# Performance work log

Measured on AMD Instinct MI355X. Metric: run time of the kernel, lower is better.

## Reference

```python
import jax, jax.numpy as jnp
import numpy as np

N_NODES = 50000
N_EDGES = 800000
D = 128


def _graph_conv(x, W, b, src, dst, n_nodes):
    """DGL GraphConv with norm='both': D_in^{-1/2} A D_out^{-1/2} X W + b."""
    ones = jnp.ones((src.shape[0],), dtype=x.dtype)
    out_deg = jax.ops.segment_sum(ones, src, num_segments=n_nodes)
    in_deg = jax.ops.segment_sum(ones, dst, num_segments=n_nodes)
    out_norm = jax.lax.rsqrt(jnp.maximum(out_deg, 1.0))  # [N]
    in_norm = jax.lax.rsqrt(jnp.maximum(in_deg, 1.0))    # [N]
    # scale src features, transform (in_feats == out_feats so order is free), aggregate
    h = (x * out_norm[:, None]) @ W                       # [N, D]
    msgs = h[src]                                         # [E, D] gather
    agg = jax.ops.segment_sum(msgs, dst, num_segments=n_nodes)  # [N, D] scatter-add
    return agg * in_norm[:, None] + b


def setup_inputs() -> dict:
    key = jax.random.key(0)
    ks = jax.random.split(key, 8)
    x = jax.random.normal(ks[0], (N_NODES, D), dtype=jnp.float32)
    src = jax.random.randint(ks[1], (N_EDGES,), 0, N_NODES, dtype=jnp.int64)
    dst = jax.random.randint(ks[2], (N_EDGES,), 0, N_NODES, dtype=jnp.int64)
    scale = 1.0 / np.sqrt(D)
    W1 = jax.random.normal(ks[3], (D, D), dtype=jnp.float32) * scale
    W2 = jax.random.normal(ks[4], (D, D), dtype=jnp.float32) * scale
    W3 = jax.random.normal(ks[5], (D, D), dtype=jnp.float32) * scale
    b1 = jnp.zeros((D,), dtype=jnp.float32)
    b2 = jnp.zeros((D,), dtype=jnp.float32)
    b3 = jnp.zeros((D,), dtype=jnp.float32)
    return {"x": x, "src": src, "dst": dst,
            "W1": W1, "b1": b1, "W2": W2, "b2": b2, "W3": W3, "b3": b3}


def reference(x, src, dst, W1, b1, W2, b2, W3, b3):
    h = _graph_conv(x, W1, b1, src, dst, N_NODES)
    h = jax.nn.relu(h)
    h = _graph_conv(h, W2, b2, src, dst, N_NODES)
    h = jax.nn.relu(h)
    h = _graph_conv(h, W3, b3, src, dst, N_NODES)
    return h
```

## Files before the change

### kernel.cpp

```cpp
#include <hip/hip_runtime.h>
#include <hip/hip_fp16.h>

#define D 128
#define HB 128
#define HT 1024
#define WMAX 12800

struct alignas(16) H8 { __half2 h[4]; };
typedef _Float16 v8h __attribute__((ext_vector_type(8)));
typedef float v4f __attribute__((ext_vector_type(4)));

__global__ __launch_bounds__(HT) void hist_kernel(const int* __restrict__ src,
                                                  const int* __restrict__ dst,
                                                  unsigned* __restrict__ partial_out,
                                                  unsigned* __restrict__ partial_in,
                                                  unsigned char* __restrict__ lrank,
                                                  int nE, int W, int epb) {
    __shared__ unsigned lcnt[WMAX];
    const bool is_dst = (blockIdx.x < HB);
    const int b = is_dst ? blockIdx.x : (blockIdx.x - HB);
    const int t = threadIdx.x;
    for (int i = t; i < W; i += HT) lcnt[i] = 0;
    __syncthreads();
    const int e0 = b * epb;
    const int e1 = min(nE, e0 + epb);
    if (is_dst) {
        for (int e = e0 + t; e < e1; e += HT) {
            const int d = dst[e];
            const unsigned sh = (unsigned)(d & 3) * 8u;
            const unsigned old = atomicAdd(&lcnt[d >> 2], 1u << sh);
            lrank[e] = (unsigned char)((old >> sh) & 0xffu);
        }
    } else {
        for (int e = e0 + t; e < e1; e += HT) {
            const int s = src[e];
            atomicAdd(&lcnt[s >> 2], 1u << ((unsigned)(s & 3) * 8u));
        }
    }
    __syncthreads();
    unsigned* g = (is_dst ? partial_in : partial_out) + (size_t)b * W;
    for (int i = t; i < W; i += HT) g[i] = lcnt[i];
}

__global__ __launch_bounds__(256) void reduce_hist_kernel(const unsigned* __restrict__ partial_out,
                                                          const unsigned* __restrict__ partial_in,
                                                          unsigned* __restrict__ offs_in,
                                                          int* __restrict__ cnt_out,
                                                          int* __restrict__ cnt_in,
                                                          int W, int n, int nbW) {
    const bool is_dst = ((int)blockIdx.x < nbW);
    const int w = (is_dst ? blockIdx.x : (blockIdx.x - nbW)) * 256 + threadIdx.x;
    if (w >= W) return;
    unsigned run = 0;
    if (is_dst) {
#pragma unroll 16
        for (int b = 0; b < HB; ++b) {
            const unsigned c = partial_in[(size_t)b * W + w];
            offs_in[(size_t)b * W + w] = run;
            run += c;
        }
    } else {
#pragma unroll 16
        for (int b = 0; b < HB; ++b) run += partial_out[(size_t)b * W + w];
    }
    int* cnt = is_dst ? cnt_in : cnt_out;
    const int n0 = w * 4;
    const int4 c4 = make_int4((int)(run & 0xffu), (int)((run >> 8) & 0xffu),
                              (int)((run >> 16) & 0xffu), (int)((run >> 24) & 0xffu));
    if (n0 + 3 < n) {
        *(int4*)&cnt[n0] = c4;
    } else {
        const int* cp = &c4.x;
        for (int i = 0; i < 4 && n0 + i < n; ++i) cnt[n0 + i] = cp[i];
    }
}

__global__ __launch_bounds__(1024) void scan_block_kernel(const int* __restrict__ deg,
                                                          int* __restrict__ rp,
                                                          int* __restrict__ bsum, int n) {
    __shared__ int wsum[16];
    const int t = threadIdx.x;
    const int lane = t & 63;
    const int wid = t >> 6;
    const int i = blockIdx.x * 1024 + t;
    const int v = (i < n) ? deg[i] : 0;
    int s = v;
#pragma unroll
    for (int off = 1; off < 64; off <<= 1) {
        int u = __shfl_up(s, off, 64);
        if (lane >= off) s += u;
    }
    if (lane == 63) wsum[wid] = s;
    __syncthreads();
    if (wid == 0) {
        int ws = (lane < 16) ? wsum[lane] : 0;
#pragma unroll
        for (int off = 1; off < 16; off <<= 1) {
            int u = __shfl_up(ws, off, 64);
            if (lane >= off) ws += u;
        }
        if (lane < 16) wsum[lane] = ws;
    }
    __syncthreads();
    const int excl = s - v + ((wid > 0) ? wsum[wid - 1] : 0);
    if (i < n) rp[i] = excl;
    if (t == 0) bsum[blockIdx.x] = wsum[15];
}

__global__ __launch_bounds__(1024) void finalize_kernel(int* __restrict__ rp,
                                                        const int* __restrict__ bsum,
                                                        const int* __restrict__ cnt_out,
                                                        const int* __restrict__ cnt_in,
                                                        float* __restrict__ onorm,
                                                        float* __restrict__ inorm,
                                                        int n, int nb, int nE) {
    __shared__ int prefix_s;
    const int t = threadIdx.x;
    if (t < 64) {
        int v = (t < nb && t < (int)blockIdx.x) ? bsum[t] : 0;
#pragma unroll
        for (int off = 1; off < 64; off <<= 1) v += __shfl_xor(v, off, 64);
        if (t == 0) prefix_s = v;
    }
    __syncthreads();
    const int i = blockIdx.x * 1024 + t;
    if (i < n) {
        rp[i] += prefix_s;
        onorm[i] = rsqrtf(fmaxf((float)cnt_out[i], 1.0f));
        inorm[i] = rsqrtf(fmaxf((float)cnt_in[i], 1.0f));
    }
    if (blockIdx.x == 0 && t == 0) rp[n] = nE;
}

__global__ void fill_csr_kernel(const int* __restrict__ src, const int* __restrict__ dst,
                                const unsigned char* __restrict__ lrank,
                                const unsigned* __restrict__ offs_in,
                                const int* __restrict__ rp,
                                int* __restrict__ srcs_sorted, int nE, int epb, int W) {
    const int e = blockIdx.x * 256 + threadIdx.x;
    if (e < nE) {
        const int d = dst[e];
        const int b = e / epb;
        const unsigned off = (offs_in[(size_t)b * W + (d >> 2)] >> ((unsigned)(d & 3) * 8u)) & 0xffu;
        srcs_sorted[rp[d] + (int)off + (int)lrank[e]] = src[e];
    }
}

__global__ __launch_bounds__(256) void prep_w_kernel(const float* __restrict__ W1,
                                                     const float* __restrict__ W2,
                                                     const float* __restrict__ W3,
                                                     _Float16* __restrict__ wt) {
    const int l = blockIdx.x;
    const float* Wsrc = (l == 0) ? W1 : ((l == 1) ? W2 : W3);
    _Float16* o = wt + (size_t)l * D * D;
    for (int i = threadIdx.x; i < D * D; i += 256) {
        const int k = i >> 7, n = i & 127;
        o[n * D + k] = (_Float16)Wsrc[i];
    }
}

template <bool EPI>
__global__ __launch_bounds__(256) void aggregate_kernel(const __half* __restrict__ xh,
                                                        const float* __restrict__ onorm,
                                                        const float* __restrict__ inorm,
                                                        const float* __restrict__ bias,
                                                        const int* __restrict__ rp,
                                                        const int* __restrict__ srcs,
                                                        __half* __restrict__ agg, int n_nodes) {
    const int node = blockIdx.x * 4 + (threadIdx.x >> 6);
    const int lane = threadIdx.x & 63;
    const int rg = lane >> 4;
    const int c8 = lane & 15;
    if (node >= n_nodes) return;
    const int e0 = rp[node];
    const int e1 = rp[node + 1];

    float acc0[8], acc1[8];
#pragma unroll
    for (int j = 0; j < 8; ++j) { acc0[j] = 0.f; acc1[j] = 0.f; }

    auto accum = [&](float* acc, const H8 v) {
#pragma unroll
        for (int j = 0; j < 4; ++j) {
            acc[2 * j]     += __low2float(v.h[j]);
            acc[2 * j + 1] += __high2float(v.h[j]);
        }
    };

    int e = e0;
    for (; e + 16 <= e1; e += 16) {
        const int s0 = srcs[e + rg];
        const int s1 = srcs[e + 4 + rg];
        const int s2 = srcs[e + 8 + rg];
        const int s3 = srcs[e + 12 + rg];
        const H8 v0 = ((const H8*)(xh + (size_t)s0 * D))[c8];
        const H8 v1 = ((const H8*)(xh + (size_t)s1 * D))[c8];
        const H8 v2 = ((const H8*)(xh + (size_t)s2 * D))[c8];
        const H8 v3 = ((const H8*)(xh + (size_t)s3 * D))[c8];
        accum(acc0, v0); accum(acc1, v1); accum(acc0, v2); accum(acc1, v3);
    }
    for (; e + 4 <= e1; e += 4) {
        const int s0 = srcs[e + rg];
        accum(acc0, ((const H8*)(xh + (size_t)s0 * D))[c8]);
    }
    if (e < e1 && rg < (e1 - e)) {
        const int s0 = srcs[e + rg];
        accum(acc1, ((const H8*)(xh + (size_t)s0 * D))[c8]);
    }

    float r[8];
#pragma unroll
    for (int j = 0; j < 8; ++j) r[j] = acc0[j] + acc1[j];
#pragma unroll
    for (int off = 16; off < 64; off <<= 1)
#pragma unroll
        for (int j = 0; j < 8; ++j) r[j] += __shfl_xor(r[j], off, 64);

    if (rg == 0) {
        if (EPI) {
            const float inm = inorm[node];
            const float onm = onorm[node];
            const float4 bv0 = ((const float4*)bias)[c8 * 2];
            const float4 bv1 = ((const float4*)bias)[c8 * 2 + 1];
            const float* bp0 = &bv0.x;
            const float* bp1 = &bv1.x;
#pragma unroll
            for (int j = 0; j < 4; ++j) {
                r[j]     = fmaxf(fmaf(r[j],     inm, bp0[j]), 0.f) * onm;
                r[j + 4] = fmaxf(fmaf(r[j + 4], inm, bp1[j]), 0.f) * onm;
            }
        }
        H8 h;
#pragma unroll
        for (int j = 0; j < 4; ++j) h.h[j] = __floats2half2_rn(r[2 * j], r[2 * j + 1]);
        ((H8*)(agg + (size_t)node * D))[c8] = h;
    }
}

template <bool A16, bool FULL, bool RELU, bool OSCALE, bool OUT16>
__global__ __launch_bounds__(256) void gemm_mfma_kernel(const void* __restrict__ Av,
                                                        const _Float16* __restrict__ Wt,
                                                        const float* __restrict__ bias,
                                                        const float* __restrict__ inorm,
                                                        const float* __restrict__ onorm,
                                                        void* __restrict__ outv, int nrows) {
    __shared__ _Float16 sA[128 * 136];
    __shared__ _Float16 sB[128 * 136];
    const int t = threadIdx.x;
    const int row0 = blockIdx.x * 128;
    const int rr = t >> 4;
    const int c8 = t & 15;

#pragma unroll
    for (int pass = 0; pass < 8; ++pass) {
        const int row = pass * 16 + rr;
        *(float4*)&sB[row * 136 + c8 * 8] = *(const float4*)&Wt[(size_t)row * D + c8 * 8];
        const int grow = row0 + row;
        if (A16) {
            float4 v = make_float4(0.f, 0.f, 0.f, 0.f);
            if (grow < nrows)
                v = *(const float4*)((const _Float16*)Av + (size_t)grow * D + c8 * 8);
            *(float4*)&sA[row * 136 + c8 * 8] = v;
        } else {
            float4 u0 = make_float4(0.f, 0.f, 0.f, 0.f);
            float4 u1 = u0;
            if (grow < nrows) {
                const float* ap = (const float*)Av + (size_t)grow * D + c8 * 8;
                u0 = ((const float4*)ap)[0];
                u1 = ((const float4*)ap)[1];
            }
            v8h hv;
            hv[0] = (_Float16)u0.x; hv[1] = (_Float16)u0.y;
            hv[2] = (_Float16)u0.z; hv[3] = (_Float16)u0.w;
            hv[4] = (_Float16)u1.x; hv[5] = (_Float16)u1.y;
            hv[6] = (_Float16)u1.z; hv[7] = (_Float16)u1.w;
            *(v8h*)&sA[row * 136 + c8 * 8] = hv;
        }
    }
    __syncthreads();

    const int w = t >> 6;
    const int lane = t & 63;
    const int m16 = lane & 15;
    const int quad = lane >> 4;

    v4f c[2][8];
#pragma unroll
    for (int rt = 0; rt < 2; ++rt)
#pragma unroll
        for (int ct = 0; ct < 8; ++ct) c[rt][ct] = (v4f){0.f, 0.f, 0.f, 0.f};

#pragma unroll
    for (int ks = 0; ks < 4; ++ks) {
        v8h afr[2], bfr[8];
#pragma unroll
        for (int rt = 0; rt < 2; ++rt)
            afr[rt] = *(const v8h*)&sA[(w * 32 + rt * 16 + m16) * 136 + ks * 32 + quad * 8];
#pragma unroll
        for (int ct = 0; ct < 8; ++ct)
            bfr[ct] = *(const v8h*)&sB[(ct * 16 + m16) * 136 + ks * 32 + quad * 8];
#pragma unroll
        for (int rt = 0; rt < 2; ++rt)
#pragma unroll
            for (int ct = 0; ct < 8; ++ct)
                c[rt][ct] = __builtin_amdgcn_mfma_f32_16x16x32_f16(afr[rt], bfr[ct], c[rt][ct], 0, 0, 0);
    }

#pragma unroll
    for (int rt = 0; rt < 2; ++rt) {
#pragma unroll
        for (int r = 0; r < 4; ++r) {
            const int row = row0 + w * 32 + rt * 16 + quad * 4 + r;
            if (row < nrows) {
                const float inm = FULL ? inorm[row] : 1.0f;
                const float osc = OSCALE ? onorm[row] : 1.0f;
#pragma unroll
                for (int ct = 0; ct < 8; ++ct) {
                    const int col = ct * 16 + m16;
                    float v = c[rt][ct][r];
                    if (FULL) v = fmaf(v, inm, bias[col]);
                    if (RELU) v = fmaxf(v, 0.f);
                    if (OSCALE) v *= osc;
                    if (OUT16) ((__half*)outv)[(size_t)row * D + col] = __float2half(v);
                    else       ((float*)outv)[(size_t)row * D + col] = v;
                }
            }
        }
    }
}

extern "C" void kernel_launch(void* const* d_in, const int* in_sizes, int n_in,
                              void* d_out, int out_size, void* d_ws, size_t ws_size,
                              hipStream_t stream) {
    const float* x   = (const float*)d_in[0];
    const int*   src = (const int*)d_in[1];
    const int*   dst = (const int*)d_in[2];
    const float* W1  = (const float*)d_in[3];
    const float* b1  = (const float*)d_in[4];
    const float* W2  = (const float*)d_in[5];
    const float* b2  = (const float*)d_in[6];
    const float* W3  = (const float*)d_in[7];
    const float* b3  = (const float*)d_in[8];

    const int N = in_sizes[0] / D;
    const int E = in_sizes[1];

    char* p = (char*)d_ws;
    auto alloc = [&](size_t bytes) -> void* {
        void* r = (void*)p;
        p += (bytes + 255) & ~(size_t)255;
        return r;
    };
    int*           cnt_out = (int*)alloc((size_t)N * 4);
    int*           cnt_in  = (int*)alloc((size_t)N * 4);
    int*           rp      = (int*)alloc((size_t)(N + 1) * 4);
    int*           bsum    = (int*)alloc(1024 * 4);
    float*         onorm   = (float*)alloc((size_t)N * 4);
    float*         inorm   = (float*)alloc((size_t)N * 4);
    int*           srcs    = (int*)alloc((size_t)E * 4);
    unsigned char* lrank   = (unsigned char*)alloc((size_t)E);
    _Float16*      wt      = (_Float16*)alloc((size_t)3 * D * D * 2);
    __half*        hbuf0   = (__half*)alloc((size_t)N * D * 2);
    __half*        hbuf1   = (__half*)alloc((size_t)N * D * 2);
    char*          scratch = (char*)alloc((size_t)3 * HB * ((N + 3) / 4) * 4);

    const int W = (N + 3) / 4;
    const int epb = (E + HB - 1) / HB;
    unsigned* partial_in  = (unsigned*)scratch;
    unsigned* partial_out = partial_in + (size_t)HB * W;
    unsigned* offs_in     = partial_out + (size_t)HB * W;
    __half*   abuf        = (__half*)scratch;
    float*    outf        = (float*)d_out;

    const int nb = (N + 1023) / 1024;
    const int nbW = (W + 255) / 256;
    const int gemmGrid = (N + 127) / 128;
    const int edgeGrid = (E + 255) / 256;
    const int aggGrid = (N + 3) / 4;

    prep_w_kernel<<<3, 256, 0, stream>>>(W1, W2, W3, wt);
    hist_kernel<<<2 * HB, HT, 0, stream>>>(src, dst, partial_out, partial_in, lrank, E, W, epb);
    reduce_hist_kernel<<<2 * nbW, 256, 0, stream>>>(partial_out, partial_in, offs_in,
                                                    cnt_out, cnt_in, W, N, nbW);
    scan_block_kernel<<<nb, 1024, 0, stream>>>(cnt_in, rp, bsum, N);
    finalize_kernel<<<nb, 1024, 0, stream>>>(rp, bsum, cnt_out, cnt_in, onorm, inorm, N, nb, E);
    fill_csr_kernel<<<edgeGrid, 256, 0, stream>>>(src, dst, lrank, offs_in, rp, srcs, E, epb, W);

    gemm_mfma_kernel<false, false, false, true, true><<<gemmGrid, 256, 0, stream>>>(
        x, wt, b1, inorm, onorm, hbuf0, N);
    aggregate_kernel<true><<<aggGrid, 256, 0, stream>>>(
        hbuf0, onorm, inorm, b1, rp, srcs, hbuf1, N);
    aggregate_kernel<false><<<aggGrid, 256, 0, stream>>>(
        hbuf1, onorm, inorm, b2, rp, srcs, abuf, N);
    gemm_mfma_kernel<true, true, true, true, true><<<gemmGrid, 256, 0, stream>>>(
        abuf, wt + (size_t)D * D, b2, inorm, onorm, hbuf0, N);
    aggregate_kernel<false><<<aggGrid, 256, 0, stream>>>(
        hbuf0, onorm, inorm, b3, rp, srcs, abuf, N);
    gemm_mfma_kernel<true, true, false, false, false><<<gemmGrid, 256, 0, stream>>>(
        abuf, wt + (size_t)2 * D * D, b3, inorm, onorm, outf, N);
}
```

Measured before the change: 262.2 us.

## Merge weight prep into histogram kernel and fuse CSR fill with first GEMM

Weight transpose/convert now runs as three extra blocks of the histogram launch, and the CSR fill runs as extra blocks inside a new 1024-thread first-layer GEMM kernel. This removes two kernel launches and lets the scatter fill overlap with the first dense transform. The new GEMM uses 16 waves per block, each computing a 16x64 tile. Output is written per element as scalar half stores instead of vectorized stores, and 1024-thread blocks with 68KB of shared memory may limit occupancy.

```diff
diff --git a/kernel.cpp b/kernel.cpp
--- a/kernel.cpp
+++ b/kernel.cpp
@@ -15,11 +15,25 @@
                                                   unsigned* __restrict__ partial_out,
                                                   unsigned* __restrict__ partial_in,
                                                   unsigned char* __restrict__ lrank,
+                                                  const float* __restrict__ W1,
+                                                  const float* __restrict__ W2,
+                                                  const float* __restrict__ W3,
+                                                  _Float16* __restrict__ wt,
                                                   int nE, int W, int epb) {
+    const int t = threadIdx.x;
+    if ((int)blockIdx.x >= 2 * HB) {
+        const int l = blockIdx.x - 2 * HB;
+        const float* Wsrc = (l == 0) ? W1 : ((l == 1) ? W2 : W3);
+        _Float16* o = wt + (size_t)l * D * D;
+        for (int i = t; i < D * D; i += HT) {
+            const int k = i >> 7, n = i & 127;
+            o[n * D + k] = (_Float16)Wsrc[i];
+        }
+        return;
+    }
     __shared__ unsigned lcnt[WMAX];
     const bool is_dst = (blockIdx.x < HB);
     const int b = is_dst ? blockIdx.x : (blockIdx.x - HB);
-    const int t = threadIdx.x;
     for (int i = t; i < W; i += HT) lcnt[i] = 0;
     __syncthreads();
     const int e0 = b * epb;
@@ -132,30 +146,85 @@
     if (blockIdx.x == 0 && t == 0) rp[n] = nE;
 }
 
-__global__ void fill_csr_kernel(const int* __restrict__ src, const int* __restrict__ dst,
-                                const unsigned char* __restrict__ lrank,
-                                const unsigned* __restrict__ offs_in,
-                                const int* __restrict__ rp,
-                                int* __restrict__ srcs_sorted, int nE, int epb, int W) {
-    const int e = blockIdx.x * 256 + threadIdx.x;
-    if (e < nE) {
-        const int d = dst[e];
-        const int b = e / epb;
-        const unsigned off = (offs_in[(size_t)b * W + (d >> 2)] >> ((unsigned)(d & 3) * 8u)) & 0xffu;
-        srcs_sorted[rp[d] + (int)off + (int)lrank[e]] = src[e];
-    }
-}
-
-__global__ __launch_bounds__(256) void prep_w_kernel(const float* __restrict__ W1,
-                                                     const float* __restrict__ W2,
-                                                     const float* __restrict__ W3,
-                                                     _Float16* __restrict__ wt) {
-    const int l = blockIdx.x;
-    const float* Wsrc = (l == 0) ? W1 : ((l == 1) ? W2 : W3);
-    _Float16* o = wt + (size_t)l * D * D;
-    for (int i = threadIdx.x; i < D * D; i += 256) {
-        const int k = i >> 7, n = i & 127;
-        o[n * D + k] = (_Float16)Wsrc[i];
+__global__ __launch_bounds__(1024) void gemm1_fill_kernel(
+    const float* __restrict__ x, const _Float16* __restrict__ wt,
+    const float* __restrict__ onorm, __half* __restrict__ y1, int nrows,
+    const int* __restrict__ src, const int* __restrict__ dst,
+    const unsigned char* __restrict__ lrank, const unsigned* __restrict__ offs_in,
+    const int* __restrict__ rp, int* __restrict__ srcs_sorted,
+    int nE, int epb, int W, int nGemmBlocks) {
+    __shared__ _Float16 sA[128 * 136];
+    __shared__ _Float16 sB[128 * 136];
+    const int t = threadIdx.x;
+
+    if ((int)blockIdx.x >= nGemmBlocks) {
+        const int e = (blockIdx.x - nGemmBlocks) * 1024 + t;
+        if (e < nE) {
+            const int d = dst[e];
+            const int b = e / epb;
+            const unsigned off =
+                (offs_in[(size_t)b * W + (d >> 2)] >> ((unsigned)(d & 3) * 8u)) & 0xffu;
+            srcs_sorted[rp[d] + (int)off + (int)lrank[e]] = src[e];
+        }
+        return;
+    }
+
+    const int row0 = blockIdx.x * 128;
+    const int rr = t >> 4;
+    const int c8 = t & 15;
+#pragma unroll
+    for (int pass = 0; pass < 2; ++pass) {
+        const int row = pass * 64 + rr;
+        *(float4*)&sB[row * 136 + c8 * 8] = *(const float4*)&wt[(size_t)row * D + c8 * 8];
+        const int grow = row0 + row;
+        float4 u0 = make_float4(0.f, 0.f, 0.f, 0.f);
+        float4 u1 = u0;
+        if (grow < nrows) {
+            const float* ap = x + (size_t)grow * D + c8 * 8;
+            u0 = ((const float4*)ap)[0];
+            u1 = ((const float4*)ap)[1];
+        }
+        v8h hv;
+        hv[0] = (_Float16)u0.x; hv[1] = (_Float16)u0.y;
+        hv[2] = (_Float16)u0.z; hv[3] = (_Float16)u0.w;
+        hv[4] = (_Float16)u1.x; hv[5] = (_Float16)u1.y;
+        hv[6] = (_Float16)u1.z; hv[7] = (_Float16)u1.w;
+        *(v8h*)&sA[row * 136 + c8 * 8] = hv;
+    }
+    __syncthreads();
+
+    const int w = t >> 6;
+    const int lane = t & 63;
+    const int m16 = lane & 15;
+    const int quad = lane >> 4;
+    const int rt = w >> 1;
+    const int ch = w & 1;
+
+    v4f c[4];
+#pragma unroll
+    for (int ct = 0; ct < 4; ++ct) c[ct] = (v4f){0.f, 0.f, 0.f, 0.f};
+
+#pragma unroll
+    for (int ks = 0; ks < 4; ++ks) {
+        const v8h a = *(const v8h*)&sA[(rt * 16 + m16) * 136 + ks * 32 + quad * 8];
+#pragma unroll
+        for (int ct = 0; ct < 4; ++ct) {
+            const v8h b = *(const v8h*)&sB[((ch * 4 + ct) * 16 + m16) * 136 + ks * 32 + quad * 8];
+            c[ct] = __builtin_amdgcn_mfma_f32_16x16x32_f16(a, b, c[ct], 0, 0, 0);
+        }
+    }
+
+#pragma unroll
+    for (int r = 0; r < 4; ++r) {
+        const int row = row0 + rt * 16 + quad * 4 + r;
+        if (row < nrows) {
+            const float osc = onorm[row];
+#pragma unroll
+            for (int ct = 0; ct < 4; ++ct) {
+                const int col = (ch * 4 + ct) * 16 + m16;
+                y1[(size_t)row * D + col] = __float2half(c[ct][r] * osc);
+            }
+        }
     }
 }
 
@@ -237,8 +306,8 @@
     }
 }
 
-template <bool A16, bool FULL, bool RELU, bool OSCALE, bool OUT16>
-__global__ __launch_bounds__(256) void gemm_mfma_kernel(const void* __restrict__ Av,
+template <bool FULL, bool RELU, bool OSCALE, bool OUT16>
+__global__ __launch_bounds__(256) void gemm_mfma_kernel(const __half* __restrict__ Ah,
                                                         const _Float16* __restrict__ Wt,
                                                         const float* __restrict__ bias,
                                                         const float* __restrict__ inorm,
@@ -256,26 +325,10 @@
         const int row = pass * 16 + rr;
         *(float4*)&sB[row * 136 + c8 * 8] = *(const float4*)&Wt[(size_t)row * D + c8 * 8];
         const int grow = row0 + row;
-        if (A16) {
-            float4 v = make_float4(0.f, 0.f, 0.f, 0.f);
-            if (grow < nrows)
-                v = *(const float4*)((const _Float16*)Av + (size_t)grow * D + c8 * 8);
-            *(float4*)&sA[row * 136 + c8 * 8] = v;
-        } else {
-            float4 u0 = make_float4(0.f, 0.f, 0.f, 0.f);
-            float4 u1 = u0;
-            if (grow < nrows) {
-                const float* ap = (const float*)Av + (size_t)grow * D + c8 * 8;
-                u0 = ((const float4*)ap)[0];
-                u1 = ((const float4*)ap)[1];
-            }
-            v8h hv;
-            hv[0] = (_Float16)u0.x; hv[1] = (_Float16)u0.y;
-            hv[2] = (_Float16)u0.z; hv[3] = (_Float16)u0.w;
-            hv[4] = (_Float16)u1.x; hv[5] = (_Float16)u1.y;
-            hv[6] = (_Float16)u1.z; hv[7] = (_Float16)u1.w;
-            *(v8h*)&sA[row * 136 + c8 * 8] = hv;
-        }
+        float4 v = make_float4(0.f, 0.f, 0.f, 0.f);
+        if (grow < nrows)
+            v = *(const float4*)((const _Float16*)Ah + (size_t)grow * D + c8 * 8);
+        *(float4*)&sA[row * 136 + c8 * 8] = v;
     }
     __syncthreads();
 
@@ -375,27 +428,28 @@
     const int nb = (N + 1023) / 1024;
     const int nbW = (W + 255) / 256;
     const int gemmGrid = (N + 127) / 128;
-    const int edgeGrid = (E + 255) / 256;
+    const int fillGrid = (E + 1023) / 1024;
     const int aggGrid = (N + 3) / 4;
 
-    prep_w_kernel<<<3, 256, 0, stream>>>(W1, W2, W3, wt);
-    hist_kernel<<<2 * HB, HT, 0, stream>>>(src, dst, partial_out, partial_in, lrank, E, W, epb);
+    hist_kernel<<<2 * HB + 3, HT, 0, stream>>>(src, dst, partial_out, partial_in, lrank,
+                                               W1, W2, W3, wt, E, W, epb);
     reduce_hist_kernel<<<2 * nbW, 256, 0, stream>>>(partial_out, partial_in, offs_in,
                                                     cnt_out, cnt_in, W, N, nbW);
     scan_block_kernel<<<nb, 1024, 0, stream>>>(cnt_in, rp, bsum, N);
     finalize_kernel<<<nb, 1024, 0, stream>>>(rp, bsum, cnt_out, cnt_in, onorm, inorm, N, nb, E);
-    fill_csr_kernel<<<edgeGrid, 256, 0, stream>>>(src, dst, lrank, offs_in, rp, srcs, E, epb, W);
-
-    gemm_mfma_kernel<false, false, false, true, true><<<gemmGrid, 256, 0, stream>>>(
-        x, wt, b1, inorm, onorm, hbuf0, N);
+
+    gemm1_fill_kernel<<<gemmGrid + fillGrid, 1024, 0, stream>>>(
+        x, wt, onorm, hbuf0, N,
+        src, dst, lrank, offs_in, rp, srcs, E, epb, W, gemmGrid);
+
     aggregate_kernel<true><<<aggGrid, 256, 0, stream>>>(
         hbuf0, onorm, inorm, b1, rp, srcs, hbuf1, N);
     aggregate_kernel<false><<<aggGrid, 256, 0, stream>>>(
         hbuf1, onorm, inorm, b2, rp, srcs, abuf, N);
-    gemm_mfma_kernel<true, true, true, true, true><<<gemmGrid, 256, 0, stream>>>(
+    gemm_mfma_kernel<true, true, true, true><<<gemmGrid, 256, 0, stream>>>(
         abuf, wt + (size_t)D * D, b2, inorm, onorm, hbuf0, N);
     aggregate_kernel<false><<<aggGrid, 256, 0, stream>>>(
         hbuf0, onorm, inorm, b3, rp, srcs, abuf, N);
-    gemm_mfma_kernel<true, true, false, false, false><<<gemmGrid, 256, 0, stream>>>(
+    gemm_mfma_kernel<true, false, false, false><<<gemmGrid, 256, 0, stream>>>(
         abuf, wt + (size_t)2 * D * D, b3, inorm, onorm, outf, N);
 }
```

Measured after the change: 245.1 us, median of 2. 6.5% less time.
